# Performance work log

Hardware: AMD Instinct MI355X
Metric: run time of the kernel (lower is better)

## Reference

```python
import jax, jax.numpy as jnp
import numpy as np

B, D, UNITS, NW = 64, 2048, 1024, 64  # batch, input_dim, units, n_weights


def _build_hash_indices(rng):
    """Replicates hash_matrix(): for each (unit j, bucket k), the (1-shifted)
    input positions i with hash(i,j) == k, padded with 0 (-> zero column)."""
    indx = rng.integers(0, NW, size=(D, UNITS))  # hash of (i, j) into [0, NW)
    counts = np.zeros((UNITS, NW), dtype=np.int64)
    for k in range(NW):
        counts[:, k] = (indx == k).sum(axis=0)
    L = int(counts.max())
    out = np.zeros((UNITS, NW, L), dtype=np.int64)
    for j in range(UNITS):
        col = indx[:, j]
        order = np.argsort(col, kind='stable')
        cnts = np.bincount(col, minlength=NW)
        splits = np.cumsum(cnts)[:-1]
        for k, part in enumerate(np.split(order, splits)):
            out[j, k, :len(part)] = part + 1  # +1 shift; 0 = padding
    return out


def setup_inputs() -> dict:
    key = jax.random.key(0)
    kx, kw = jax.random.split(key)
    x = jax.random.normal(kx, (B, D), dtype=jnp.float32)
    w = jax.random.normal(kw, (NW,), dtype=jnp.float32) * 0.05  # random_normal_initializer
    b = jnp.zeros((UNITS,), dtype=jnp.float32)
    indices = jnp.asarray(_build_hash_indices(np.random.default_rng(2)))
    return {"x": x, "w": w, "b": b, "indices": indices}


def reference(x, w, b, indices):
    # prepend a zero column so padding index 0 gathers 0.0
    x_cat = jnp.pad(x, ((0, 0), (1, 0)))                 # [B, D+1]
    gathered = jnp.take(x_cat, indices, axis=1)          # [B, UNITS, NW, L]
    reduced = gathered.sum(axis=-1)                      # [B, UNITS, NW]
    return jnp.einsum('buk,k->bu', reduced, w) + b       # [B, UNITS]
```

## Files before the change

### kernel.cpp

```cpp
#include <hip/hip_runtime.h>


#define B_DIM   64
#define D_DIM   2048
#define D4      (D_DIM / 4)
#define UNITS_N 1024
#define NW_N    64
#define U_PER_BLOCK 4
#define THREADS 1024
#define PAIRS_PER_WAVE 16

__global__ __launch_bounds__(THREADS, 4)
void EfficientHashedLinear_72043781423546_kernel(
    const float* __restrict__ x,
    const float* __restrict__ w,
    const float* __restrict__ bias,
    const int*   __restrict__ indices,
    float*       __restrict__ out,
    int L)
{
    __shared__ float rows[U_PER_BLOCK][D_DIM];
    __shared__ float w_lds[NW_N];

    const int tid  = threadIdx.x;
    const int wave = tid >> 6;
    const int lane = tid & 63;
    const int u0   = blockIdx.x * U_PER_BLOCK;

    {
        float4* r4 = (float4*)rows;
        const float4 z = make_float4(0.f, 0.f, 0.f, 0.f);
        #pragma unroll
        for (int i = tid; i < U_PER_BLOCK * D4; i += THREADS)
            r4[i] = z;
        if (tid < NW_N) w_lds[tid] = w[tid];
    }
    __syncthreads();

    int idxv[PAIRS_PER_WAVE];
    #pragma unroll
    for (int p = 0; p < PAIRS_PER_WAVE; ++p) {
        const int pair = wave * PAIRS_PER_WAVE + p;
        const int uu   = pair >> 6;
        const int k    = pair & 63;
        const int* bp  = indices + ((size_t)(u0 + uu) * NW_N + k) * L;
        idxv[p] = (lane < L) ? bp[lane] : 0;
    }
    #pragma unroll
    for (int p = 0; p < PAIRS_PER_WAVE; ++p) {
        const int pair = wave * PAIRS_PER_WAVE + p;
        const int uu   = pair >> 6;
        const int k    = pair & 63;
        if (idxv[p] > 0) rows[uu][idxv[p] - 1] = w_lds[k];
    }
    if (L > 64) {
        #pragma unroll 1
        for (int p = 0; p < PAIRS_PER_WAVE; ++p) {
            const int pair = wave * PAIRS_PER_WAVE + p;
            const int uu   = pair >> 6;
            const int k    = pair & 63;
            const int* bp  = indices + ((size_t)(u0 + uu) * NW_N + k) * L;
            const float wk = w_lds[k];
            for (int l = 64 + lane; l < L; l += 64) {
                int idx = bp[l];
                if (idx > 0) rows[uu][idx - 1] = wk;
            }
        }
    }
    __syncthreads();

    const int b0 = wave * 4;
    const float4* x4 = (const float4*)x;

    float acc[4][U_PER_BLOCK];
    #pragma unroll
    for (int bj = 0; bj < 4; ++bj)
        #pragma unroll
        for (int uu = 0; uu < U_PER_BLOCK; ++uu)
            acc[bj][uu] = 0.0f;

    #pragma unroll 1
    for (int step = 0; step < D4 / 64; ++step) {
        const int i4 = step * 64 + lane;
        float4 rv[U_PER_BLOCK];
        #pragma unroll
        for (int uu = 0; uu < U_PER_BLOCK; ++uu)
            rv[uu] = ((const float4*)rows[uu])[i4];
        #pragma unroll
        for (int bj = 0; bj < 4; ++bj) {
            const float4 xv = x4[(b0 + bj) * D4 + i4];
            #pragma unroll
            for (int uu = 0; uu < U_PER_BLOCK; ++uu) {
                acc[bj][uu] += xv.x * rv[uu].x;
                acc[bj][uu] += xv.y * rv[uu].y;
                acc[bj][uu] += xv.z * rv[uu].z;
                acc[bj][uu] += xv.w * rv[uu].w;
            }
        }
    }

    #pragma unroll
    for (int bj = 0; bj < 4; ++bj) {
        #pragma unroll
        for (int uu = 0; uu < U_PER_BLOCK; ++uu) {
            float v = acc[bj][uu];
            #pragma unroll
            for (int off = 32; off > 0; off >>= 1)
                v += __shfl_down(v, off, 64);
            if (lane == 0)
                out[(b0 + bj) * UNITS_N + (u0 + uu)] = v + bias[u0 + uu];
        }
    }
}

extern "C" void kernel_launch(void* const* d_in, const int* in_sizes, int n_in,
                              void* d_out, int out_size, void* d_ws, size_t ws_size,
                              hipStream_t stream) {
    const float* x       = (const float*)d_in[0];
    const float* w       = (const float*)d_in[1];
    const float* bias    = (const float*)d_in[2];
    const int*   indices = (const int*)d_in[3];
    float*       out     = (float*)d_out;

    const int L = in_sizes[3] / (UNITS_N * NW_N);

    dim3 grid(UNITS_N / U_PER_BLOCK);
    dim3 block(THREADS);
    EfficientHashedLinear_72043781423546_kernel<<<grid, block, 0, stream>>>(
        x, w, bias, indices, out, L);
}
```

Before: 81.26 us.

## Halve units per block, prefetch x rows into registers, overlap with scatter

Each block now handles 2 units with 512 threads instead of 4 with 1024, giving 512 blocks instead of 256 and half the LDS per block. Each wave covers 8 batch rows, and their first x tile is loaded before the scatter barrier so global latency overlaps the LDS row build. The main loop software-pipelines x loads one step ahead. The trade-off is more register pressure from 8 rows of prefetch buffers and lower x reuse per block, so x is re-read from global memory twice as often.

```diff
diff --git a/kernel.cpp b/kernel.cpp
--- a/kernel.cpp
+++ b/kernel.cpp
@@ -6,9 +6,12 @@
 #define D4      (D_DIM / 4)
 #define UNITS_N 1024
 #define NW_N    64
-#define U_PER_BLOCK 4
-#define THREADS 1024
-#define PAIRS_PER_WAVE 16
+#define U_PER_BLOCK 2
+#define THREADS 512
+#define WAVES   (THREADS / 64)
+#define PAIRS_PER_WAVE (U_PER_BLOCK * NW_N / WAVES)
+#define ROWS_PER_WAVE  (B_DIM / WAVES)
+#define STEPS   (D4 / 64)
 
 __global__ __launch_bounds__(THREADS, 4)
 void EfficientHashedLinear_72043781423546_kernel(
@@ -35,7 +38,6 @@
             r4[i] = z;
         if (tid < NW_N) w_lds[tid] = w[tid];
     }
-    __syncthreads();
 
     int idxv[PAIRS_PER_WAVE];
     #pragma unroll
@@ -46,6 +48,16 @@
         const int* bp  = indices + ((size_t)(u0 + uu) * NW_N + k) * L;
         idxv[p] = (lane < L) ? bp[lane] : 0;
     }
+
+    const int b0 = wave * ROWS_PER_WAVE;
+    const float4* x4 = (const float4*)x;
+    float4 xc[ROWS_PER_WAVE];
+    #pragma unroll
+    for (int bj = 0; bj < ROWS_PER_WAVE; ++bj)
+        xc[bj] = x4[(b0 + bj) * D4 + lane];
+
+    __syncthreads();
+
     #pragma unroll
     for (int p = 0; p < PAIRS_PER_WAVE; ++p) {
         const int pair = wave * PAIRS_PER_WAVE + p;
@@ -69,38 +81,45 @@
     }
     __syncthreads();
 
-    const int b0 = wave * 4;
-    const float4* x4 = (const float4*)x;
-
-    float acc[4][U_PER_BLOCK];
+    float acc[ROWS_PER_WAVE][U_PER_BLOCK];
     #pragma unroll
-    for (int bj = 0; bj < 4; ++bj)
+    for (int bj = 0; bj < ROWS_PER_WAVE; ++bj)
         #pragma unroll
         for (int uu = 0; uu < U_PER_BLOCK; ++uu)
             acc[bj][uu] = 0.0f;
 
-    #pragma unroll 1
-    for (int step = 0; step < D4 / 64; ++step) {
+    #pragma unroll 2
+    for (int step = 0; step < STEPS; ++step) {
         const int i4 = step * 64 + lane;
+        float4 xn[ROWS_PER_WAVE];
+        if (step + 1 < STEPS) {
+            #pragma unroll
+            for (int bj = 0; bj < ROWS_PER_WAVE; ++bj)
+                xn[bj] = x4[(b0 + bj) * D4 + (i4 + 64)];
+        }
         float4 rv[U_PER_BLOCK];
         #pragma unroll
         for (int uu = 0; uu < U_PER_BLOCK; ++uu)
             rv[uu] = ((const float4*)rows[uu])[i4];
         #pragma unroll
-        for (int bj = 0; bj < 4; ++bj) {
-            const float4 xv = x4[(b0 + bj) * D4 + i4];
+        for (int bj = 0; bj < ROWS_PER_WAVE; ++bj) {
             #pragma unroll
             for (int uu = 0; uu < U_PER_BLOCK; ++uu) {
-                acc[bj][uu] += xv.x * rv[uu].x;
-                acc[bj][uu] += xv.y * rv[uu].y;
-                acc[bj][uu] += xv.z * rv[uu].z;
-                acc[bj][uu] += xv.w * rv[uu].w;
+                acc[bj][uu] += xc[bj].x * rv[uu].x;
+                acc[bj][uu] += xc[bj].y * rv[uu].y;
+                acc[bj][uu] += xc[bj].z * rv[uu].z;
+                acc[bj][uu] += xc[bj].w * rv[uu].w;
             }
+        }
+        if (step + 1 < STEPS) {
+            #pragma unroll
+            for (int bj = 0; bj < ROWS_PER_WAVE; ++bj)
+                xc[bj] = xn[bj];
         }
     }
 
     #pragma unroll
-    for (int bj = 0; bj < 4; ++bj) {
+    for (int bj = 0; bj < ROWS_PER_WAVE; ++bj) {
         #pragma unroll
         for (int uu = 0; uu < U_PER_BLOCK; ++uu) {
             float v = acc[bj][uu];
```

Measured after the change: 150.9 us. +85.7%, slower.
